# Optimization experiments

Measured on AMD Instinct MI355X. Metric: run time of the kernel, lower is better.

## Reference

```python
import jax, jax.numpy as jnp
import numpy as np

EPS = 1e-6
H = 12  # num_attention_heads

def _phi(x):
    # feature map used by fast-transformers LinearAttention: elu(x) + 1
    return jax.nn.elu(x) + 1.0

def setup_inputs() -> dict:
    key = jax.random.key(0)
    k1, k2, k3 = jax.random.split(key, 3)
    B, N, D = 32, 1024, 768
    x = jax.random.normal(k1, (B, N, D), dtype=jnp.float32)
    W_qkv = jax.random.normal(k2, (D, 3 * D), dtype=jnp.float32) * (D ** -0.5)
    W_out = jax.random.normal(k3, (D, D), dtype=jnp.float32) * (D ** -0.5)
    b_out = jnp.zeros((D,), dtype=jnp.float32)
    return {"x": x, "W_qkv": W_qkv, "W_out": W_out, "b_out": b_out}

def reference(x, W_qkv, W_out, b_out):
    B, N, D = x.shape
    d = D // H
    # F.pad(x, [0,0,0,1]): append one zero token along sequence
    x_ = jnp.pad(x, ((0, 0), (0, 1), (0, 0)))              # [B, N+1, D]
    qkv = x_ @ W_qkv                                        # [B, N+1, 3D]
    q, k, v = jnp.split(qkv, 3, axis=-1)
    q = q.reshape(B, N + 1, H, d)
    k = k.reshape(B, N + 1, H, d)
    v = v.reshape(B, N + 1, H, d)
    # non-causal linear attention (mask is all-ones -> no masking)
    q = _phi(q)
    k = _phi(k)
    kv = jnp.einsum('bshd,bshm->bhdm', k, v)                # [B, H, d, d]
    z = 1.0 / (jnp.einsum('blhd,bhd->blh', q, k.sum(axis=1)) + EPS)
    out = jnp.einsum('blhd,bhdm,blh->blhm', q, kv, z)       # [B, N+1, H, d]
    out = out.reshape(B, N + 1, D)
    out = out @ W_out + b_out                               # dropout = identity (eval)
    return out[:, :-1, :]                                   # drop padding token
```

## Files before the change

kernel.cpp:

```cpp
#include <hip/hip_runtime.h>
#include <hip/hip_bf16.h>


typedef __bf16 bf16x8 __attribute__((ext_vector_type(8)));
typedef float f32x4 __attribute__((ext_vector_type(4)));

#define SBAR  __builtin_amdgcn_sched_barrier(0)

__device__ __forceinline__ ushort f2bf(float f) {
  union { float f; unsigned u; } x; x.f = f;
  unsigned r = x.u + 0x7fffu + ((x.u >> 16) & 1u);
  return (ushort)(r >> 16);
}
__device__ __forceinline__ float bf2f(ushort h) {
  union { unsigned u; float f; } x; x.u = ((unsigned)h) << 16;
  return x.f;
}
__device__ __forceinline__ float bits2f(unsigned u) {
  union { unsigned u; float f; } x; x.u = u;
  return x.f;
}
__device__ __forceinline__ void gload_lds16(const void* g, void* lds) {
  __builtin_amdgcn_global_load_lds((const __attribute__((address_space(1))) void*)g,
                                   (__attribute__((address_space(3))) void*)lds, 16, 0, 0);
}

__global__ __launch_bounds__(256) void cvt_f32_bf16(const float* __restrict__ in,
                                                    ushort* __restrict__ out, int n4) {
  int i = blockIdx.x * 256 + threadIdx.x;
  if (i >= n4) return;
  float4 v = reinterpret_cast<const float4*>(in)[i];
  ushort4 o;
  o.x = f2bf(v.x); o.y = f2bf(v.y); o.z = f2bf(v.z); o.w = f2bf(v.w);
  reinterpret_cast<ushort4*>(out)[i] = o;
}

__global__ __launch_bounds__(256) void transpose_cvt2(const float* __restrict__ srcA,
                                                      ushort* __restrict__ dstA,
                                                      const float* __restrict__ srcB,
                                                      ushort* __restrict__ dstB) {
  const float* src; ushort* dst; int R, C;
  if (blockIdx.z == 0) { src = srcA; dst = dstA; R = 768; C = 2304; }
  else                 { if (blockIdx.x >= 24) return; src = srcB; dst = dstB; R = 768; C = 768; }
  __shared__ float tile[32][33];
  int bc = blockIdx.x * 32, br = blockIdx.y * 32;
  int tx = threadIdx.x & 31, ty = threadIdx.x >> 5;
  #pragma unroll
  for (int i = 0; i < 32; i += 8)
    tile[ty + i][tx] = src[(size_t)(br + ty + i) * C + (bc + tx)];
  __syncthreads();
  #pragma unroll
  for (int i = 0; i < 32; i += 8)
    dst[(size_t)(bc + ty + i) * R + (br + tx)] = f2bf(tile[tx][ty + i]);
}

template <int MODE>
__global__ __launch_bounds__(512, 4) void gemm3b(const ushort* __restrict__ A,
                                                 const ushort* __restrict__ Bt,
                                                 void* __restrict__ C,
                                                 const float* __restrict__ bias,
                                                 int N, int K, int nbx, int cpx) {
  extern __shared__ ushort lds[];
  const int tid = threadIdx.x;
  const int lane = tid & 63;
  const int wid = tid >> 6;
  const int wm = wid >> 2, wn = wid & 3;
  const int laneR = lane & 15, laneS = lane >> 4;

  const int bid = blockIdx.x;
  const int lin = (bid & 7) * cpx + (bid >> 3);
  const int by = lin / nbx, bx = lin - by * nbx;
  const int m0 = by * 128, n0 = bx * 256;
  const int NT = K >> 5;

  const int sr = tid >> 2, ss = tid & 3;
  const int sslot = ss ^ ((sr >> 1) & 3);
  const ushort* Asrc = A + (size_t)(m0 + sr) * K + sslot * 8;
  const ushort* Bsrc = Bt + (size_t)(n0 + sr) * K + sslot * 8;
  const size_t rowstep128 = (size_t)128 * K;
  const int ldstA = tid * 8;
  const int ldstB = 4096 + tid * 8;

  const int sprime = laneS ^ ((laneR >> 1) & 3);
  const int aoff = (wm * 64 + laneR) * 32 + sprime * 8;
  const int boff = 4096 + (wn * 64 + laneR) * 32 + sprime * 8;

  f32x4 acc[4][4] = {};

  #define STAGE_T(KT, DB)                                                         \
    { gload_lds16(Asrc + (KT) * 32, lds + (DB) + ldstA);                          \
      gload_lds16(Bsrc + (KT) * 32, lds + (DB) + ldstB);                          \
      gload_lds16(Bsrc + (KT) * 32 + rowstep128, lds + (DB) + ldstB + 4096); }

  STAGE_T(0, 0);
  STAGE_T(1, 12288);
  asm volatile("s_waitcnt vmcnt(3)" ::: "memory");
  SBAR;
  __builtin_amdgcn_s_barrier();
  SBAR;

  for (int t = 0; t < NT; ++t) {
    const ushort* cb = lds + (t % 3) * 12288;
    const int db2 = ((t + 2) % 3) * 12288;
    const int t2 = (t + 2 < NT) ? t + 2 : t;
    bf16x8 a[4], b[4];
    #pragma unroll
    for (int j = 0; j < 4; ++j) b[j] = *(const bf16x8*)(cb + boff + j * 512);
    #pragma unroll
    for (int i = 0; i < 4; ++i) a[i] = *(const bf16x8*)(cb + aoff + i * 512);
    STAGE_T(t2, db2);
    asm volatile("s_waitcnt vmcnt(3)" ::: "memory");
    SBAR;
    __builtin_amdgcn_s_barrier();
    SBAR;
    __builtin_amdgcn_s_setprio(1);
    #pragma unroll
    for (int i = 0; i < 4; ++i)
      #pragma unroll
      for (int j = 0; j < 4; ++j)
        acc[i][j] = __builtin_amdgcn_mfma_f32_16x16x32_bf16(a[i], b[j], acc[i][j], 0, 0, 0);
    __builtin_amdgcn_s_setprio(0);
    SBAR;
    __builtin_amdgcn_s_barrier();
    SBAR;
  }
  #undef STAGE_T
  asm volatile("s_waitcnt vmcnt(0)" ::: "memory");

  #pragma unroll
  for (int i = 0; i < 4; ++i) {
    const int grow0 = m0 + wm * 64 + i * 16 + (laneS << 2);
    #pragma unroll
    for (int j = 0; j < 4; ++j) {
      const int gcol = n0 + wn * 64 + j * 16 + laneR;
      #pragma unroll
      for (int r = 0; r < 4; ++r) {
        float v = acc[i][j][r];
        if (MODE == 0) {
          if (gcol < 1536) v = (v > 0.f) ? (v + 1.f) : __expf(v);
          reinterpret_cast<ushort*>(C)[(size_t)(grow0 + r) * N + gcol] = f2bf(v);
        } else {
          reinterpret_cast<float*>(C)[(size_t)(grow0 + r) * N + gcol] = v + bias[gcol];
        }
      }
    }
  }
}

__global__ __launch_bounds__(256) void kv_partial(const ushort* __restrict__ qkv,
                                                  float* __restrict__ kv_part,
                                                  float* __restrict__ ks_part) {
  const int blk = blockIdx.x;
  const int bh = blk >> 2, sp = blk & 3;
  const int b = bh / 12, h = bh % 12;
  const int tid = threadIdx.x;
  __shared__ float Ks[32 * 68];
  __shared__ float Vs[32 * 68];
  float acc[4][4] = {};
  float kacc[4] = {};
  const int dq0 = (tid & 15) * 4, mq0 = (tid >> 4) * 4;
  const int r = tid >> 3, o = (tid & 7) * 8;
  for (int st = 0; st < 256; st += 32) {
    const size_t rowbase = (size_t)(b * 1024 + sp * 256 + st + r) * 2304 + h * 64 + o;
    int4 kraw = *reinterpret_cast<const int4*>(qkv + rowbase + 768);
    int4 vraw = *reinterpret_cast<const int4*>(qkv + rowbase + 1536);
    float kf[8], vf[8];
    {
      const unsigned* kw = reinterpret_cast<const unsigned*>(&kraw);
      const unsigned* vw = reinterpret_cast<const unsigned*>(&vraw);
      #pragma unroll
      for (int w = 0; w < 4; ++w) {
        kf[2 * w]     = bits2f(kw[w] << 16);
        kf[2 * w + 1] = bits2f(kw[w] & 0xffff0000u);
        vf[2 * w]     = bits2f(vw[w] << 16);
        vf[2 * w + 1] = bits2f(vw[w] & 0xffff0000u);
      }
    }
    __syncthreads();
    #pragma unroll
    for (int w = 0; w < 8; ++w) {
      Ks[r * 68 + o + w] = kf[w];
      Vs[r * 68 + o + w] = vf[w];
    }
    __syncthreads();
    #pragma unroll 8
    for (int s = 0; s < 32; ++s) {
      f32x4 kk = *reinterpret_cast<const f32x4*>(&Ks[s * 68 + dq0]);
      f32x4 vv = *reinterpret_cast<const f32x4*>(&Vs[s * 68 + mq0]);
      #pragma unroll
      for (int jm = 0; jm < 4; ++jm)
        #pragma unroll
        for (int id = 0; id < 4; ++id)
          acc[jm][id] += vv[jm] * kk[id];
      if (mq0 == 0) {
        #pragma unroll
        for (int id = 0; id < 4; ++id) kacc[id] += kk[id];
      }
    }
  }
  float* kvp = kv_part + ((size_t)sp * 384 + bh) * 4096;
  #pragma unroll
  for (int jm = 0; jm < 4; ++jm)
    #pragma unroll
    for (int id = 0; id < 4; ++id)
      kvp[(mq0 + jm) * 64 + dq0 + id] = acc[jm][id];
  if (mq0 == 0) {
    #pragma unroll
    for (int id = 0; id < 4; ++id)
      ks_part[((size_t)sp * 384 + bh) * 64 + dq0 + id] = kacc[id];
  }
}

__global__ __launch_bounds__(256) void kv_reduce(const float* __restrict__ kv_part,
                                                 const float* __restrict__ ks_part,
                                                 ushort* __restrict__ kv_bf,
                                                 float* __restrict__ ksum) {
  int i = blockIdx.x * 256 + threadIdx.x;
  if (i < 384 * 4096) {
    float s = 0.f;
    #pragma unroll
    for (int p = 0; p < 4; ++p) s += kv_part[(size_t)p * (384 * 4096) + i];
    kv_bf[i] = f2bf(s);
  }
  if (i < 384 * 64) {
    float s = 1.0f;
    #pragma unroll
    for (int p = 0; p < 4; ++p) s += ks_part[(size_t)p * (384 * 64) + i];
    ksum[i] = s;
  }
}

__global__ __launch_bounds__(256) void attn_kernel(const ushort* __restrict__ qkv,
                                                   const ushort* __restrict__ kv_bf,
                                                   const float* __restrict__ ksum,
                                                   ushort* __restrict__ attn) {
  const int blk = blockIdx.x;
  const int bh = blk >> 3, tb = blk & 7;
  const int b = bh / 12, h = bh % 12;
  const int row0 = b * 1024 + tb * 128;
  __shared__ ushort Qs[128 * 64];
  __shared__ ushort KVs[64 * 64];
  __shared__ float zs[128];
  __shared__ float ks_lds[64];
  const int tid = threadIdx.x;
  const int lane = tid & 63, w = tid >> 6;
  #pragma unroll
  for (int j = 0; j < 4; ++j) {
    int c = j * 256 + tid;
    int qr = c >> 3, dsl = c & 7;
    int ssl = dsl ^ (qr & 7);
    gload_lds16(qkv + (size_t)(row0 + qr) * 2304 + h * 64 + ssl * 8, &Qs[c * 8]);
  }
  #pragma unroll
  for (int j = 0; j < 2; ++j) {
    int c = j * 256 + tid;
    int mr = c >> 3, dsl = c & 7;
    int ssl = dsl ^ (mr & 7);
    gload_lds16(kv_bf + (size_t)bh * 4096 + mr * 64 + ssl * 8, &KVs[c * 8]);
  }
  if (tid < 64) ks_lds[tid] = ksum[bh * 64 + tid];
  asm volatile("s_waitcnt vmcnt(0)" ::: "memory");
  __syncthreads();
  if (tid < 128) {
    float d = 0.f;
    const int tx7 = tid & 7;
    #pragma unroll
    for (int s = 0; s < 8; ++s) {
      int4 raw = *reinterpret_cast<const int4*>(&Qs[tid * 64 + ((s ^ tx7) << 3)]);
      const unsigned* wds = reinterpret_cast<const unsigned*>(&raw);
      #pragma unroll
      for (int w2 = 0; w2 < 4; ++w2) {
        d += bits2f(wds[w2] << 16) * ks_lds[s * 8 + 2 * w2];
        d += bits2f(wds[w2] & 0xffff0000u) * ks_lds[s * 8 + 2 * w2 + 1];
      }
    }
    zs[tid] = 1.f / (d + 1e-6f);
  }
  __syncthreads();
  f32x4 acc[2][4] = {};
  const int lr7 = (lane & 15) & 7;
  #pragma unroll
  for (int ks = 0; ks < 2; ++ks) {
    const int sxor = ((ks * 4 + (lane >> 4)) ^ lr7) << 3;
    bf16x8 a[2], bb[4];
    #pragma unroll
    for (int i = 0; i < 2; ++i)
      a[i] = *reinterpret_cast<const bf16x8*>(&Qs[(w * 32 + i * 16 + (lane & 15)) * 64 + sxor]);
    #pragma unroll
    for (int j = 0; j < 4; ++j)
      bb[j] = *reinterpret_cast<const bf16x8*>(&KVs[(j * 16 + (lane & 15)) * 64 + sxor]);
    #pragma unroll
    for (int i = 0; i < 2; ++i)
      #pragma unroll
      for (int j = 0; j < 4; ++j)
        acc[i][j] = __builtin_amdgcn_mfma_f32_16x16x32_bf16(a[i], bb[j], acc[i][j], 0, 0, 0);
  }
  #pragma unroll
  for (int i = 0; i < 2; ++i) {
    const int t0 = w * 32 + i * 16 + ((lane >> 4) << 2);
    #pragma unroll
    for (int j = 0; j < 4; ++j) {
      const int m = j * 16 + (lane & 15);
      #pragma unroll
      for (int r = 0; r < 4; ++r) {
        float v = acc[i][j][r] * zs[t0 + r];
        attn[(size_t)(row0 + t0 + r) * 768 + h * 64 + m] = f2bf(v);
      }
    }
  }
}

extern "C" void kernel_launch(void* const* d_in, const int* in_sizes, int n_in,
                              void* d_out, int out_size, void* d_ws, size_t ws_size,
                              hipStream_t stream) {
  (void)in_sizes; (void)n_in; (void)out_size; (void)ws_size;
  const float* x    = (const float*)d_in[0];
  const float* Wqkv = (const float*)d_in[1];
  const float* Wout = (const float*)d_in[2];
  const float* bout = (const float*)d_in[3];
  float* out = (float*)d_out;
  char* ws = (char*)d_ws;

  ushort* xbf    = (ushort*)(ws);
  ushort* wqkvT  = (ushort*)(ws + 50331648);
  ushort* woutT  = (ushort*)(ws + 53870592);
  ushort* qkv    = (ushort*)(ws + 55050240);
  float*  ksp    = (float*) (ws + 206045184);
  ushort* kvbf   = (ushort*)(ws + 206438400);
  float*  ksum   = (float*) (ws + 209584128);
  float*  kvpart = (float*)(ws);
  ushort* attn   = (ushort*)(ws);

  static const int LDS3 = 73728;
  hipFuncSetAttribute(reinterpret_cast<const void*>(&gemm3b<0>),
                      hipFuncAttributeMaxDynamicSharedMemorySize, LDS3);
  hipFuncSetAttribute(reinterpret_cast<const void*>(&gemm3b<1>),
                      hipFuncAttributeMaxDynamicSharedMemorySize, LDS3);

  cvt_f32_bf16<<<24576, 256, 0, stream>>>(x, xbf, 6291456);
  transpose_cvt2<<<dim3(72, 24, 2), 256, 0, stream>>>(Wqkv, wqkvT, Wout, woutT);
  gemm3b<0><<<2304, 512, LDS3, stream>>>(xbf, wqkvT, qkv, nullptr, 2304, 768, 9, 288);
  kv_partial<<<1536, 256, 0, stream>>>(qkv, kvpart, ksp);
  kv_reduce<<<6144, 256, 0, stream>>>(kvpart, ksp, kvbf, ksum);
  attn_kernel<<<3072, 256, 0, stream>>>(qkv, kvbf, ksum, attn);
  gemm3b<1><<<768, 512, LDS3, stream>>>(attn, woutT, out, bout, 768, 768, 3, 96);
}
```

Measured before the change: 290.4 us.

## Fuse KV partial sums and reduction into one full-sequence kernel per head

```diff
diff --git a/kernel.cpp b/kernel.cpp
--- a/kernel.cpp
+++ b/kernel.cpp
@@ -147,11 +147,10 @@
   }
 }
 
-__global__ __launch_bounds__(256) void kv_partial(const ushort* __restrict__ qkv,
-                                                  float* __restrict__ kv_part,
-                                                  float* __restrict__ ks_part) {
-  const int blk = blockIdx.x;
-  const int bh = blk >> 2, sp = blk & 3;
+__global__ __launch_bounds__(256) void kv_full(const ushort* __restrict__ qkv,
+                                               ushort* __restrict__ kv_bf,
+                                               float* __restrict__ ksum) {
+  const int bh = blockIdx.x;
   const int b = bh / 12, h = bh % 12;
   const int tid = threadIdx.x;
   __shared__ float Ks[32 * 68];
@@ -160,8 +159,8 @@
   float kacc[4] = {};
   const int dq0 = (tid & 15) * 4, mq0 = (tid >> 4) * 4;
   const int r = tid >> 3, o = (tid & 7) * 8;
-  for (int st = 0; st < 256; st += 32) {
-    const size_t rowbase = (size_t)(b * 1024 + sp * 256 + st + r) * 2304 + h * 64 + o;
+  for (int st = 0; st < 1024; st += 32) {
+    const size_t rowbase = (size_t)(b * 1024 + st + r) * 2304 + h * 64 + o;
     int4 kraw = *reinterpret_cast<const int4*>(qkv + rowbase + 768);
     int4 vraw = *reinterpret_cast<const int4*>(qkv + rowbase + 1536);
     float kf[8], vf[8];
@@ -198,35 +197,16 @@
       }
     }
   }
-  float* kvp = kv_part + ((size_t)sp * 384 + bh) * 4096;
+  ushort* kvp = kv_bf + (size_t)bh * 4096;
   #pragma unroll
   for (int jm = 0; jm < 4; ++jm)
     #pragma unroll
     for (int id = 0; id < 4; ++id)
-      kvp[(mq0 + jm) * 64 + dq0 + id] = acc[jm][id];
+      kvp[(mq0 + jm) * 64 + dq0 + id] = f2bf(acc[jm][id]);
   if (mq0 == 0) {
     #pragma unroll
     for (int id = 0; id < 4; ++id)
-      ks_part[((size_t)sp * 384 + bh) * 64 + dq0 + id] = kacc[id];
-  }
-}
-
-__global__ __launch_bounds__(256) void kv_reduce(const float* __restrict__ kv_part,
-                                                 const float* __restrict__ ks_part,
-                                                 ushort* __restrict__ kv_bf,
-                                                 float* __restrict__ ksum) {
-  int i = blockIdx.x * 256 + threadIdx.x;
-  if (i < 384 * 4096) {
-    float s = 0.f;
-    #pragma unroll
-    for (int p = 0; p < 4; ++p) s += kv_part[(size_t)p * (384 * 4096) + i];
-    kv_bf[i] = f2bf(s);
-  }
-  if (i < 384 * 64) {
-    float s = 1.0f;
-    #pragma unroll
-    for (int p = 0; p < 4; ++p) s += ks_part[(size_t)p * (384 * 64) + i];
-    ksum[i] = s;
+      ksum[(size_t)bh * 64 + dq0 + id] = kacc[id] + 1.0f;
   }
 }
 
@@ -325,10 +305,8 @@
   ushort* wqkvT  = (ushort*)(ws + 50331648);
   ushort* woutT  = (ushort*)(ws + 53870592);
   ushort* qkv    = (ushort*)(ws + 55050240);
-  float*  ksp    = (float*) (ws + 206045184);
   ushort* kvbf   = (ushort*)(ws + 206438400);
   float*  ksum   = (float*) (ws + 209584128);
-  float*  kvpart = (float*)(ws);
   ushort* attn   = (ushort*)(ws);
 
   static const int LDS3 = 73728;
@@ -340,8 +318,7 @@
   cvt_f32_bf16<<<24576, 256, 0, stream>>>(x, xbf, 6291456);
   transpose_cvt2<<<dim3(72, 24, 2), 256, 0, stream>>>(Wqkv, wqkvT, Wout, woutT);
   gemm3b<0><<<2304, 512, LDS3, stream>>>(xbf, wqkvT, qkv, nullptr, 2304, 768, 9, 288);
-  kv_partial<<<1536, 256, 0, stream>>>(qkv, kvpart, ksp);
-  kv_reduce<<<6144, 256, 0, stream>>>(kvpart, ksp, kvbf, ksum);
+  kv_full<<<384, 256, 0, stream>>>(qkv, kvbf, ksum);
   attn_kernel<<<3072, 256, 0, stream>>>(qkv, kvbf, ksum, attn);
   gemm3b<1><<<768, 512, LDS3, stream>>>(attn, woutT, out, bout, 768, 768, 3, 96);
 }
```

Measured after the change: 303.8 us. 4.6% more time.
